# Performance work log

Measured on AMD Instinct MI355X. Metric: run time of the kernel, lower is better.

The kernel has to match this reference:

```python
import jax, jax.numpy as jnp
import numpy as np

N = 100000
E = 1600000
IN_DIM = 128
HID_DIM = 128
OUT_DIM = 128


def _gcn_conv(x, W, b, row, col, n):
    # PyG GCNConv: x' = D^{-1/2} (A + I) D^{-1/2} (x W) + b, self-loops included
    xw = x @ W  # [n, dout]
    deg = jnp.zeros((n,), xw.dtype).at[col].add(1.0)  # in-degree incl self-loops
    dinv = jnp.where(deg > 0, jax.lax.rsqrt(deg), 0.0)
    norm = dinv[row] * dinv[col]  # [e]
    msg = xw[row] * norm[:, None]  # [e, dout] -- dominant memory traffic
    out = jax.ops.segment_sum(msg, col, num_segments=n)
    return out + b


def setup_inputs() -> dict:
    key = jax.random.key(0)
    k1, k2, k3, k4, k5, k6 = jax.random.split(key, 6)
    posts = jax.random.normal(k1, (N, IN_DIM), dtype=jnp.float32)
    edge_index = jax.random.randint(k2, (2, E), 0, N, dtype=jnp.int64)
    W1 = jax.random.normal(k3, (IN_DIM, HID_DIM), dtype=jnp.float32) * (1.0 / np.sqrt(IN_DIM))
    b1 = jnp.zeros((HID_DIM,), dtype=jnp.float32)
    W2 = jax.random.normal(k4, (HID_DIM + IN_DIM, OUT_DIM), dtype=jnp.float32) * (1.0 / np.sqrt(HID_DIM + IN_DIM))
    b2 = jnp.zeros((OUT_DIM,), dtype=jnp.float32)
    return {"posts": posts, "W1": W1, "b1": b1, "W2": W2, "b2": b2,
            "edge_index": edge_index, "rootIndex": 0}


def reference(posts, W1, b1, W2, b2, edge_index, rootIndex):
    n = posts.shape[0]
    loops = jnp.arange(n, dtype=edge_index.dtype)
    row = jnp.concatenate([edge_index[0], loops])
    col = jnp.concatenate([edge_index[1], loops])

    conv1_out = _gcn_conv(posts, W1, b1, row, col, n)  # [n, hid]
    post_root = jnp.broadcast_to(posts[rootIndex], (n, posts.shape[1]))
    conv1_root = jnp.broadcast_to(conv1_out[rootIndex], (n, conv1_out.shape[1]))

    conv2_in = jax.nn.relu(jnp.concatenate([conv1_out, post_root], axis=1))
    # dropout is identity at inference
    conv2_out = jax.nn.relu(_gcn_conv(conv2_in, W2, b2, row, col, n))

    feature = jnp.concatenate([conv1_root, conv2_out], axis=1)  # [n, hid+out]
    # avg_pool1d(kernel_size=3, stride=1) over the feature axis -> [n, hid+out-2]
    pooled = (feature[:, :-2] + feature[:, 1:-1] + feature[:, 2:]) * (1.0 / 3.0)
    return pooled
```

## Files before the change

kernel.cpp:

```cpp
#include <hip/hip_runtime.h>
#include <hip/hip_fp16.h>

#define DIM 128
#define CSTRIDE 64
#define BSHIFT 9
#define MAXBE 9216
typedef _Float16 half8 __attribute__((ext_vector_type(8)));
typedef float f32x4 __attribute__((ext_vector_type(4)));

__global__ void k_wprep(const float* __restrict__ W1, const float* __restrict__ W2,
                        __half* __restrict__ Wf1h, __half* __restrict__ Wf2h,
                        int* __restrict__ bucketCur){
  const float* Wsrc = (blockIdx.x < 8) ? W1 : W2;
  _Float16* Wf = (_Float16*)((blockIdx.x < 8) ? Wf1h : Wf2h);
  int id   = (blockIdx.x & 7)*256 + threadIdx.x;
  int lane = id & 63;
  int ckc  = id >> 6;
  int kc   = ckc & 3, ct = ckc >> 2;
  int kbase = kc*32 + (lane >> 4)*8;
  int c     = ct*16 + (lane & 15);
  half8 v;
  #pragma unroll
  for (int i = 0; i < 8; i++)
    v[i] = (_Float16)Wsrc[(size_t)(kbase + i)*DIM + c];
  *(half8*)(Wf + (size_t)id*8) = v;
  if (blockIdx.x == 0) bucketCur[threadIdx.x] = 0;
}

template<int INH>
__device__ __forceinline__ void gemm_mfma(const void* __restrict__ Xv,
    const _Float16* __restrict__ Wf, const float* __restrict__ addvec,
    const int* __restrict__ cntp, __half* __restrict__ Yh, int N, int doRelu, int gb){
  int wid = threadIdx.x >> 6;
  int l   = threadIdx.x & 63;
  int g   = l >> 4;
  int lr  = l & 15;
  int rowA = gb*64 + wid*16 + lr;
  int rA   = (rowA < N) ? rowA : (N - 1);

  f32x4 acc[8];
  #pragma unroll
  for (int ct = 0; ct < 8; ct++) acc[ct] = (f32x4){0.f, 0.f, 0.f, 0.f};

  #pragma unroll
  for (int kc = 0; kc < 4; kc++){
    half8 a;
    if (INH){
      a = *(const half8*)((const _Float16*)Xv + (size_t)rA*DIM + kc*32 + g*8);
    } else {
      const float* xp = (const float*)Xv + (size_t)rA*DIM + kc*32 + g*8;
      float4 x0 = *(const float4*)xp;
      float4 x1 = *(const float4*)(xp + 4);
      a[0]=(_Float16)x0.x; a[1]=(_Float16)x0.y; a[2]=(_Float16)x0.z; a[3]=(_Float16)x0.w;
      a[4]=(_Float16)x1.x; a[5]=(_Float16)x1.y; a[6]=(_Float16)x1.z; a[7]=(_Float16)x1.w;
    }
    if (doRelu){
      #pragma unroll
      for (int i = 0; i < 8; i++) a[i] = (a[i] > (_Float16)0.f) ? a[i] : (_Float16)0.f;
    }
    #pragma unroll
    for (int ct = 0; ct < 8; ct++){
      half8 b = *(const half8*)(Wf + ((size_t)(ct*4 + kc)*64 + l)*8);
      acc[ct] = __builtin_amdgcn_mfma_f32_16x16x32_f16(a, b, acc[ct], 0, 0, 0);
    }
  }

  int m0 = gb*64 + wid*16 + g*4;
  float av[8];
  #pragma unroll
  for (int ct = 0; ct < 8; ct++) av[ct] = addvec ? addvec[ct*16 + lr] : 0.f;
  #pragma unroll
  for (int r = 0; r < 4; r++){
    int rr = m0 + r;
    if (rr < N){
      float dv = cntp ? rsqrtf((float)(cntp[rr] + 1)) : 1.f;
      #pragma unroll
      for (int ct = 0; ct < 8; ct++){
        float o = dv*(acc[ct][r] + av[ct]);
        Yh[(size_t)rr*DIM + ct*16 + lr] = __float2half(o);
      }
    }
  }
}

__global__ __launch_bounds__(256) void k_megaB(const float* __restrict__ posts,
    const __half* __restrict__ Wf1, __half* __restrict__ xw1u,
    const int* __restrict__ row, const int* __restrict__ col, int E,
    int* __restrict__ bucketCur, uint2* __restrict__ spair, int N, int nG, int nCB){
  __shared__ int hist[256];
  __shared__ int sbase[256];
  int bid = blockIdx.x;
  int m = bid % 3;
  if (m < 2){
    int g = (bid/3)*2 + m;
    if (g < nG)
      gemm_mfma<0>(posts, (const _Float16*)Wf1, nullptr, nullptr, xw1u, N, 0, g);
  } else {
    int cb = bid / 3;
    if (cb >= nCB) return;
    int t = threadIdx.x;
    hist[t] = 0;
    __syncthreads();
    int base_e = cb*2048 + t;
    int bq[8], lr[8], rq[8], cq[8];
    #pragma unroll
    for (int q = 0; q < 8; q++){
      int e = base_e + q*256;
      if (e < E){
        cq[q] = col[e];
        rq[q] = row[e];
        bq[q] = cq[q] >> BSHIFT;
        lr[q] = atomicAdd(&hist[bq[q]], 1);
      } else bq[q] = -1;
    }
    __syncthreads();
    int h = hist[t];
    if (h > 0) sbase[t] = atomicAdd(&bucketCur[t], h);
    __syncthreads();
    #pragma unroll
    for (int q = 0; q < 8; q++){
      if (bq[q] >= 0){
        int p = sbase[bq[q]] + lr[q];
        if (p < MAXBE)
          spair[(size_t)bq[q]*MAXBE + p] = make_uint2((unsigned)rq[q], (unsigned)cq[q]);
      }
    }
  }
}

__global__ __launch_bounds__(256) void k_build(const uint2* __restrict__ spair,
    const int* __restrict__ bucketCur, int* __restrict__ csrp,
    int* __restrict__ cnt, int N){
  __shared__ int c512[512];
  int b = blockIdx.x;
  int t = threadIdx.x;
  c512[t] = 0; c512[t + 256] = 0;
  __syncthreads();
  int nb = bucketCur[b]; if (nb > MAXBE) nb = MAXBE;
  const uint2* sp = spair + (size_t)b*MAXBE;
  for (int i = t; i < nb; i += 256){
    uint2 pr = sp[i];
    int c = (int)pr.y;
    int rank = atomicAdd(&c512[c & 511], 1);
    if (rank < CSTRIDE)
      csrp[(size_t)c*CSTRIDE + rank] = (int)pr.x;
  }
  __syncthreads();
  int n0 = (b << BSHIFT) + t;
  if (n0 < N) cnt[n0] = c512[t];
  int n1 = n0 + 256;
  if (n1 < ((b + 1) << BSHIFT) && n1 < N) cnt[n1] = c512[t + 256];
}

__global__ __launch_bounds__(256) void k_megaC(const __half* __restrict__ c1h,
    const __half* __restrict__ Wf2, const float* __restrict__ cvec,
    const int* __restrict__ cnt, __half* __restrict__ xw2s,
    const float* __restrict__ cpool, float* __restrict__ outp, int N, int nG, int nF){
  int bid = blockIdx.x;
  if (bid < nG){
    gemm_mfma<1>(c1h, (const _Float16*)Wf2, cvec, cnt, xw2s, N, 1, bid);
  } else {
    int f = bid - nG;
    if (f >= nF) return;
    int total = N * 63;
    #pragma unroll
    for (int i = 0; i < 8; i++){
      int w = f*2048 + i*256 + threadIdx.x;
      if (w < total){
        unsigned int r  = (unsigned int)w / 63u;
        unsigned int c2 = (unsigned int)w - r*63u;
        float2 val = *(const float2*)(cpool + c2*2);
        *(float2*)(outp + (size_t)r*254 + c2*2) = val;
      }
    }
  }
}

__global__ void k_conv1(const __half* __restrict__ xw1u, const int* __restrict__ csrp,
                        const int* __restrict__ cnt,
                        const float* __restrict__ b, const int* __restrict__ rootIdx,
                        __half* __restrict__ outh, float* __restrict__ c1root, int N){
  int wid  = (blockIdx.x*blockDim.x + threadIdx.x) >> 6;
  if (wid >= N) return;
  int lane = threadIdx.x & 63;
  int half = lane >> 5;
  int sl   = lane & 31;
  int v = wid;
  float dv = rsqrtf((float)(cnt[v] + 1));
  long long o0 = (long long)v * CSTRIDE;
  int total = cnt[v] + 1;

  __half2 a01 = __float2half2_rn(0.f), a23 = __float2half2_rn(0.f);
  const __half* base = xw1u;

  auto idx = [&](int t){ return (t == 0) ? v : csrp[o0 + t - 1]; };
  auto dhv = [&](int r){ return __float2half_rn(rsqrtf((float)(cnt[r] + 1))); };
  auto accum = [&](uint2 wv, __half dh){
    __half2 d2 = __half2half2(dh);
    a01 = __hfma2(*(__half2*)&wv.x, d2, a01);
    a23 = __hfma2(*(__half2*)&wv.y, d2, a23);
  };

  int j = half;
  if (j + 14 < total){
    int nid[8];
    #pragma unroll
    for (int q = 0; q < 8; q++) nid[q] = idx(j + 2*q);
    while (j + 14 < total){
      int cur[8];
      #pragma unroll
      for (int q = 0; q < 8; q++) cur[q] = nid[q];
      int jn = j + 16;
      if (jn + 14 < total){
        #pragma unroll
        for (int q = 0; q < 8; q++) nid[q] = csrp[o0 + jn + 2*q - 1];
      }
      uint2 u[8]; __half dh[8];
      #pragma unroll
      for (int q = 0; q < 8; q++){
        u[q]  = *(const uint2*)(base + (size_t)cur[q]*DIM + sl*4);
        dh[q] = dhv(cur[q]);
      }
      #pragma unroll
      for (int q = 0; q < 8; q++) accum(u[q], dh[q]);
      j = jn;
    }
  }
  while (j + 6 < total){
    int i0 = idx(j), i1 = idx(j+2), i2 = idx(j+4), i3 = idx(j+6);
    uint2 u0 = *(const uint2*)(base + (size_t)i0*DIM + sl*4);
    uint2 u1 = *(const uint2*)(base + (size_t)i1*DIM + sl*4);
    uint2 u2 = *(const uint2*)(base + (size_t)i2*DIM + sl*4);
    uint2 u3 = *(const uint2*)(base + (size_t)i3*DIM + sl*4);
    __half d0 = dhv(i0), d1 = dhv(i1), d2 = dhv(i2), d3 = dhv(i3);
    accum(u0, d0); accum(u1, d1); accum(u2, d2); accum(u3, d3);
    j += 8;
  }
  for (; j < total; j += 2){
    int r = idx(j);
    uint2 u = *(const uint2*)(base + (size_t)r*DIM + sl*4);
    accum(u, dhv(r));
  }

  int r01 = __shfl_xor(*(int*)&a01, 32);
  int r23 = __shfl_xor(*(int*)&a23, 32);
  a01 = __hadd2(a01, *(__half2*)&r01);
  a23 = __hadd2(a23, *(__half2*)&r23);

  if (half == 0){
    float2 f01 = __half22float2(a01), f23 = __half22float2(a23);
    float4 bb = *(const float4*)(b + sl*4);
    float rx = dv*f01.x + bb.x, ry = dv*f01.y + bb.y;
    float rz = dv*f23.x + bb.z, rw = dv*f23.y + bb.w;
    __half2 h01 = __floats2half2_rn(rx, ry);
    __half2 h23 = __floats2half2_rn(rz, rw);
    uint2 u = make_uint2(*(unsigned int*)&h01, *(unsigned int*)&h23);
    *(uint2*)(outh + (size_t)v*DIM + sl*4) = u;
    if (v == rootIdx[0])
      *(float4*)(c1root + sl*4) = make_float4(rx, ry, rz, rw);
  }
}

__global__ void k_small(const float* __restrict__ posts, const float* __restrict__ W2,
                        const float* __restrict__ c1root, const int* __restrict__ rootIdx,
                        float* __restrict__ cvec, float* __restrict__ cpool){
  int j = threadIdx.x;
  int root = rootIdx[0];
  __shared__ float pr[DIM];
  __shared__ float cr[DIM];
  pr[j] = fmaxf(posts[(size_t)root*DIM + j], 0.f);
  cr[j] = c1root[j];
  __syncthreads();
  float s = 0.f;
  #pragma unroll 4
  for (int k = 0; k < DIM; k++) s += pr[k] * W2[(size_t)(DIM + k)*DIM + j];
  cvec[j] = s;
  cpool[j] = (j < 126) ? (cr[j] + cr[j+1] + cr[j+2]) * (1.f/3.f) : cr[j];
}

__global__ void k_conv2(const __half* __restrict__ xws, const int* __restrict__ csrp,
                        const int* __restrict__ cnt,
                        const float* __restrict__ b2,
                        const float* __restrict__ cpool, float* __restrict__ out, int N){
  int wid  = (blockIdx.x*blockDim.x + threadIdx.x) >> 6;
  if (wid >= N) return;
  int lane = threadIdx.x & 63;
  int half = lane >> 5;
  int sl   = lane & 31;
  int v = wid;
  float dv = rsqrtf((float)(cnt[v] + 1));
  long long o0 = (long long)v * CSTRIDE;
  int total = cnt[v] + 1;

  __half2 a01 = __float2half2_rn(0.f), a23 = __float2half2_rn(0.f);
  const __half* base = xws;

  auto idx = [&](int t){ return (t == 0) ? v : csrp[o0 + t - 1]; };
  auto accum = [&](uint2 wv){
    a01 = __hadd2(a01, *(__half2*)&wv.x);
    a23 = __hadd2(a23, *(__half2*)&wv.y);
  };

  int j = half;
  if (j + 14 < total){
    int nid[8];
    #pragma unroll
    for (int q = 0; q < 8; q++) nid[q] = idx(j + 2*q);
    while (j + 14 < total){
      int cur[8];
      #pragma unroll
      for (int q = 0; q < 8; q++) cur[q] = nid[q];
      int jn = j + 16;
      if (jn + 14 < total){
        #pragma unroll
        for (int q = 0; q < 8; q++) nid[q] = csrp[o0 + jn + 2*q - 1];
      }
      uint2 u[8];
      #pragma unroll
      for (int q = 0; q < 8; q++) u[q] = *(const uint2*)(base + (size_t)cur[q]*DIM + sl*4);
      #pragma unroll
      for (int q = 0; q < 8; q++) accum(u[q]);
      j = jn;
    }
  }
  while (j + 6 < total){
    int i0 = idx(j), i1 = idx(j+2), i2 = idx(j+4), i3 = idx(j+6);
    uint2 u0 = *(const uint2*)(base + (size_t)i0*DIM + sl*4);
    uint2 u1 = *(const uint2*)(base + (size_t)i1*DIM + sl*4);
    uint2 u2 = *(const uint2*)(base + (size_t)i2*DIM + sl*4);
    uint2 u3 = *(const uint2*)(base + (size_t)i3*DIM + sl*4);
    accum(u0); accum(u1); accum(u2); accum(u3);
    j += 8;
  }
  for (; j < total; j += 2){
    uint2 u = *(const uint2*)(base + (size_t)idx(j)*DIM + sl*4);
    accum(u);
  }

  int r01 = __shfl_xor(*(int*)&a01, 32);
  int r23 = __shfl_xor(*(int*)&a23, 32);
  a01 = __hadd2(a01, *(__half2*)&r01);
  a23 = __hadd2(a23, *(__half2*)&r23);

  if (half == 0){
    float2 f01 = __half22float2(a01), f23 = __half22float2(a23);
    float4 bb = *(const float4*)(b2 + sl*4);
    float o0v = fmaxf(dv*f01.x + bb.x, 0.f);
    float o1v = fmaxf(dv*f01.y + bb.y, 0.f);
    float o2v = fmaxf(dv*f23.x + bb.z, 0.f);
    float o3v = fmaxf(dv*f23.y + bb.w, 0.f);

    float pz = __shfl_up(o2v, 1);
    float pw = __shfl_up(o3v, 1);
    if (sl == 0){ pz = cpool[126]; pw = cpool[127]; }
    const float third = 1.f/3.f;
    float q0 = (pz + pw + o0v) * third;
    float q1 = (pw + o0v + o1v) * third;
    float q2 = (o0v + o1v + o2v) * third;
    float q3 = (o1v + o2v + o3v) * third;

    float* orow = out + (size_t)v*254;
    *(float2*)(orow + 126 + sl*4)     = make_float2(q0, q1);
    *(float2*)(orow + 126 + sl*4 + 2) = make_float2(q2, q3);
  }
}

extern "C" void kernel_launch(void* const* d_in, const int* in_sizes, int n_in,
                              void* d_out, int out_size, void* d_ws, size_t ws_size,
                              hipStream_t stream){
  const float* posts = (const float*)d_in[0];
  const float* W1    = (const float*)d_in[1];
  const float* b1    = (const float*)d_in[2];
  const float* W2    = (const float*)d_in[3];
  const float* b2    = (const float*)d_in[4];
  const int*   eidx  = (const int*)d_in[5];
  const int*   rootI = (const int*)d_in[6];
  int N = in_sizes[0] / DIM;
  int E = in_sizes[5] / 2;
  const int* row = eidx;
  const int* col = eidx + E;

  char* p = (char*)d_ws;
  auto alloc = [&](size_t bytes)->void*{
    void* q = (void*)p; p += (bytes + 255) & ~(size_t)255; return q;
  };
  __half* xw1u  = (__half*)alloc((size_t)N*DIM*2);
  __half* xw2s  = (__half*)alloc((size_t)N*DIM*2);
  __half* c1h   = (__half*)alloc((size_t)N*DIM*2);
  __half* Wf1   = (__half*)alloc((size_t)DIM*DIM*2);
  __half* Wf2   = (__half*)alloc((size_t)DIM*DIM*2);
  float* c1root = (float*)alloc(DIM*4);
  float* cvec   = (float*)alloc(DIM*4);
  float* cpool  = (float*)alloc(DIM*4);
  int*   cnt    = (int*)alloc((size_t)N*4);
  int*   csrp   = (int*)alloc((size_t)N*CSTRIDE*4);
  int*   bCur   = (int*)alloc(256*4);
  int    NBUCK  = (N + (1 << BSHIFT) - 1) >> BSHIFT;
  uint2* spair  = (uint2*)alloc((size_t)NBUCK*MAXBE*8);

  int nG  = (N + 63) / 64;
  int nCB = (E + 2047) / 2048;
  int q3  = ((nG + 1)/2 > nCB) ? (nG + 1)/2 : nCB;
  int nF  = (N*63 + 2047) / 2048;

  k_wprep<<<16, 256, 0, stream>>>(W1, W2, Wf1, Wf2, bCur);
  k_megaB<<<3*q3, 256, 0, stream>>>(posts, Wf1, xw1u, row, col, E, bCur, spair, N, nG, nCB);
  k_build<<<NBUCK, 256, 0, stream>>>(spair, bCur, csrp, cnt, N);
  k_conv1<<<(N + 3)/4, 256, 0, stream>>>(xw1u, csrp, cnt, b1, rootI, c1h, c1root, N);
  k_small<<<1, 128, 0, stream>>>(posts, W2, c1root, rootI, cvec, cpool);
  k_megaC<<<nG + nF, 256, 0, stream>>>(c1h, Wf2, cvec, cnt, xw2s, cpool,
                                       (float*)d_out, N, nG, nF);
  k_conv2<<<(N + 3)/4, 256, 0, stream>>>(xw2s, csrp, cnt, b2, cpool,
                                         (float*)d_out, N);
}
```

Measured before the change: 241.0 us.

## Compute root conv1 separately and overlap conv1 second half with conv2 GEMM

A single-block kernel now computes the root node's conv1 output, cvec and cpool directly, removing the dependency of k_small on the full conv1 pass. Conv1 is split into two halves: the first half runs alongside the output pool fill, and the second half is interleaved in one launch with the GEMM tiles for the already-finished first half of nodes. A final small launch does the remaining GEMM tiles. The intent is to overlap the gather-bound aggregation with MFMA GEMM work and drop one launch boundary. The cost is an extra launch, a serial single-block root kernel, and extra complexity in how blocks are split across kernels.

```diff
diff --git a/kernel.cpp b/kernel.cpp
--- a/kernel.cpp
+++ b/kernel.cpp
@@ -152,40 +152,48 @@
   if (n1 < ((b + 1) << BSHIFT) && n1 < N) cnt[n1] = c512[t + 256];
 }
 
-__global__ __launch_bounds__(256) void k_megaC(const __half* __restrict__ c1h,
-    const __half* __restrict__ Wf2, const float* __restrict__ cvec,
-    const int* __restrict__ cnt, __half* __restrict__ xw2s,
-    const float* __restrict__ cpool, float* __restrict__ outp, int N, int nG, int nF){
-  int bid = blockIdx.x;
-  if (bid < nG){
-    gemm_mfma<1>(c1h, (const _Float16*)Wf2, cvec, cnt, xw2s, N, 1, bid);
-  } else {
-    int f = bid - nG;
-    if (f >= nF) return;
-    int total = N * 63;
-    #pragma unroll
-    for (int i = 0; i < 8; i++){
-      int w = f*2048 + i*256 + threadIdx.x;
-      if (w < total){
-        unsigned int r  = (unsigned int)w / 63u;
-        unsigned int c2 = (unsigned int)w - r*63u;
-        float2 val = *(const float2*)(cpool + c2*2);
-        *(float2*)(outp + (size_t)r*254 + c2*2) = val;
-      }
-    }
-  }
-}
-
-__global__ void k_conv1(const __half* __restrict__ xw1u, const int* __restrict__ csrp,
-                        const int* __restrict__ cnt,
-                        const float* __restrict__ b, const int* __restrict__ rootIdx,
-                        __half* __restrict__ outh, float* __restrict__ c1root, int N){
-  int wid  = (blockIdx.x*blockDim.x + threadIdx.x) >> 6;
-  if (wid >= N) return;
+__global__ void k_root(const __half* __restrict__ xw1u, const int* __restrict__ csrp,
+                       const int* __restrict__ cnt, const float* __restrict__ b1,
+                       const float* __restrict__ posts, const float* __restrict__ W2,
+                       const int* __restrict__ rootIdx,
+                       float* __restrict__ cvec, float* __restrict__ cpool){
+  __shared__ float cr[DIM];
+  __shared__ float pr[DIM];
+  int t = threadIdx.x;
+  int root = rootIdx[0];
+  int rc = cnt[root];
+  float dvr = rsqrtf((float)(rc + 1));
+  const int* lst = csrp + (size_t)root*CSTRIDE;
+  float a = __half2float(xw1u[(size_t)root*DIM + t]) * dvr;
+  int i = 0;
+  for (; i + 4 <= rc; i += 4){
+    int r0 = lst[i], r1 = lst[i+1], r2 = lst[i+2], r3 = lst[i+3];
+    float f0 = __half2float(xw1u[(size_t)r0*DIM + t]) * rsqrtf((float)(cnt[r0] + 1));
+    float f1 = __half2float(xw1u[(size_t)r1*DIM + t]) * rsqrtf((float)(cnt[r1] + 1));
+    float f2 = __half2float(xw1u[(size_t)r2*DIM + t]) * rsqrtf((float)(cnt[r2] + 1));
+    float f3 = __half2float(xw1u[(size_t)r3*DIM + t]) * rsqrtf((float)(cnt[r3] + 1));
+    a += (f0 + f1) + (f2 + f3);
+  }
+  for (; i < rc; i++){
+    int r = lst[i];
+    a += __half2float(xw1u[(size_t)r*DIM + t]) * rsqrtf((float)(cnt[r] + 1));
+  }
+  cr[t] = dvr*a + b1[t];
+  pr[t] = fmaxf(posts[(size_t)root*DIM + t], 0.f);
+  __syncthreads();
+  float s = 0.f;
+  #pragma unroll 4
+  for (int k = 0; k < DIM; k++) s += pr[k] * W2[(size_t)(DIM + k)*DIM + t];
+  cvec[t] = s;
+  cpool[t] = (t < 126) ? (cr[t] + cr[t+1] + cr[t+2]) * (1.f/3.f) : cr[t];
+}
+
+__device__ __forceinline__ void conv1_work(int v, const __half* __restrict__ xw1u,
+    const int* __restrict__ csrp, const int* __restrict__ cnt,
+    const float* __restrict__ b, __half* __restrict__ outh){
   int lane = threadIdx.x & 63;
   int half = lane >> 5;
   int sl   = lane & 31;
-  int v = wid;
   float dv = rsqrtf((float)(cnt[v] + 1));
   long long o0 = (long long)v * CSTRIDE;
   int total = cnt[v] + 1;
@@ -256,26 +264,59 @@
     __half2 h23 = __floats2half2_rn(rz, rw);
     uint2 u = make_uint2(*(unsigned int*)&h01, *(unsigned int*)&h23);
     *(uint2*)(outh + (size_t)v*DIM + sl*4) = u;
-    if (v == rootIdx[0])
-      *(float4*)(c1root + sl*4) = make_float4(rx, ry, rz, rw);
-  }
-}
-
-__global__ void k_small(const float* __restrict__ posts, const float* __restrict__ W2,
-                        const float* __restrict__ c1root, const int* __restrict__ rootIdx,
-                        float* __restrict__ cvec, float* __restrict__ cpool){
-  int j = threadIdx.x;
-  int root = rootIdx[0];
-  __shared__ float pr[DIM];
-  __shared__ float cr[DIM];
-  pr[j] = fmaxf(posts[(size_t)root*DIM + j], 0.f);
-  cr[j] = c1root[j];
-  __syncthreads();
-  float s = 0.f;
-  #pragma unroll 4
-  for (int k = 0; k < DIM; k++) s += pr[k] * W2[(size_t)(DIM + k)*DIM + j];
-  cvec[j] = s;
-  cpool[j] = (j < 126) ? (cr[j] + cr[j+1] + cr[j+2]) * (1.f/3.f) : cr[j];
+  }
+}
+
+__global__ __launch_bounds__(256) void k_conv1a(const __half* __restrict__ xw1u,
+    const int* __restrict__ csrp, const int* __restrict__ cnt,
+    const float* __restrict__ b, __half* __restrict__ c1h,
+    const float* __restrict__ cpool, float* __restrict__ outp,
+    int N, int Nh, int nCv1, int nF){
+  int bid = blockIdx.x;
+  if (bid < nCv1){
+    int v = bid*4 + (threadIdx.x >> 6);
+    if (v < Nh) conv1_work(v, xw1u, csrp, cnt, b, c1h);
+  } else {
+    int f = bid - nCv1;
+    if (f >= nF) return;
+    int total = N * 63;
+    #pragma unroll
+    for (int i = 0; i < 8; i++){
+      int w = f*2048 + i*256 + threadIdx.x;
+      if (w < total){
+        unsigned int r  = (unsigned int)w / 63u;
+        unsigned int c2 = (unsigned int)w - r*63u;
+        float2 val = *(const float2*)(cpool + c2*2);
+        *(float2*)(outp + (size_t)r*254 + c2*2) = val;
+      }
+    }
+  }
+}
+
+__global__ __launch_bounds__(256) void k_megaD(const __half* __restrict__ xw1u,
+    const int* __restrict__ csrp, const int* __restrict__ cnt,
+    const float* __restrict__ b, __half* __restrict__ c1h,
+    const __half* __restrict__ Wf2, const float* __restrict__ cvec,
+    __half* __restrict__ xw2s, int N, int Nh, int nCv2, int nGa){
+  int bid = blockIdx.x;
+  int m = bid % 17;
+  if (m < 16){
+    int cb = (bid/17)*16 + m;
+    if (cb < nCv2){
+      int v = Nh + cb*4 + (threadIdx.x >> 6);
+      if (v < N) conv1_work(v, xw1u, csrp, cnt, b, c1h);
+    }
+  } else {
+    int g = bid / 17;
+    if (g < nGa)
+      gemm_mfma<1>(c1h, (const _Float16*)Wf2, cvec, cnt, xw2s, N, 1, g);
+  }
+}
+
+__global__ __launch_bounds__(256) void k_megaC2(const __half* __restrict__ c1h,
+    const __half* __restrict__ Wf2, const float* __restrict__ cvec,
+    const int* __restrict__ cnt, __half* __restrict__ xw2s, int N, int gb0){
+  gemm_mfma<1>(c1h, (const _Float16*)Wf2, cvec, cnt, xw2s, N, 1, gb0 + blockIdx.x);
 }
 
 __global__ void k_conv2(const __half* __restrict__ xws, const int* __restrict__ csrp,
@@ -389,7 +430,6 @@
   __half* c1h   = (__half*)alloc((size_t)N*DIM*2);
   __half* Wf1   = (__half*)alloc((size_t)DIM*DIM*2);
   __half* Wf2   = (__half*)alloc((size_t)DIM*DIM*2);
-  float* c1root = (float*)alloc(DIM*4);
   float* cvec   = (float*)alloc(DIM*4);
   float* cpool  = (float*)alloc(DIM*4);
   int*   cnt    = (int*)alloc((size_t)N*4);
@@ -403,13 +443,23 @@
   int q3  = ((nG + 1)/2 > nCB) ? (nG + 1)/2 : nCB;
   int nF  = (N*63 + 2047) / 2048;
 
+  int Nh   = ((N/2 + 63)/64)*64;
+  if (Nh > N) Nh = (N/64)*64;
+  int nCv1 = (Nh + 3)/4;
+  int nCv2 = (N - Nh + 3)/4;
+  int nGa  = Nh/64;
+  int nGb  = (N - Nh + 63)/64;
+  int q17  = ((nCv2 + 15)/16 > nGa) ? (nCv2 + 15)/16 : nGa;
+
   k_wprep<<<16, 256, 0, stream>>>(W1, W2, Wf1, Wf2, bCur);
   k_megaB<<<3*q3, 256, 0, stream>>>(posts, Wf1, xw1u, row, col, E, bCur, spair, N, nG, nCB);
   k_build<<<NBUCK, 256, 0, stream>>>(spair, bCur, csrp, cnt, N);
-  k_conv1<<<(N + 3)/4, 256, 0, stream>>>(xw1u, csrp, cnt, b1, rootI, c1h, c1root, N);
-  k_small<<<1, 128, 0, stream>>>(posts, W2, c1root, rootI, cvec, cpool);
-  k_megaC<<<nG + nF, 256, 0, stream>>>(c1h, Wf2, cvec, cnt, xw2s, cpool,
-                                       (float*)d_out, N, nG, nF);
+  k_root <<<1, 128, 0, stream>>>(xw1u, csrp, cnt, b1, posts, W2, rootI, cvec, cpool);
+  k_conv1a<<<nCv1 + nF, 256, 0, stream>>>(xw1u, csrp, cnt, b1, c1h, cpool,
+                                          (float*)d_out, N, Nh, nCv1, nF);
+  k_megaD<<<17*q17, 256, 0, stream>>>(xw1u, csrp, cnt, b1, c1h, Wf2, cvec,
+                                      xw2s, N, Nh, nCv2, nGa);
+  k_megaC2<<<nGb, 256, 0, stream>>>(c1h, Wf2, cvec, cnt, xw2s, N, nGa);
   k_conv2<<<(N + 3)/4, 256, 0, stream>>>(xw2s, csrp, cnt, b2, cpool,
                                          (float*)d_out, N);
 }
```

New measurement: 272.6 us. +13.1%, slower.
